# Performance work log

Hardware: AMD Instinct MI355X
Metric: run time of the kernel (lower is better)

The kernel has to match this reference:

```python
import jax, jax.numpy as jnp
import numpy as np

N, DN, DE, L, FE = 1024, 128, 128, 4, 5

def setup_inputs() -> dict:
    key = jax.random.key(0)
    ks = jax.random.split(key, 20)
    f = lambda k, shape, fan: jax.random.normal(k, shape, dtype=jnp.float32) / np.sqrt(fan)
    h = jax.random.normal(ks[0], (1, N, DN), dtype=jnp.float32)
    e = jax.random.normal(ks[1], (1, N, N, DE), dtype=jnp.float32)
    adj = (jax.random.uniform(ks[2], (1, N, N)) < 0.03).astype(jnp.float32)  # sparse-ish dense adjacency
    edge = jax.random.normal(ks[3], (FE,), dtype=jnp.float32)
    return {
        'h': h, 'e': e, 'adj': adj, 'edge': edge,
        # message linear over concat(h_j, e_ij), split into node/edge parts
        'w_msg_h': f(ks[4], (DN, DN), DN + DE),
        'w_msg_e': f(ks[5], (DN, DE), DN + DE),
        'b_msg':   jnp.zeros((DN,), jnp.float32),
        # GRUCell params (torch layout: gates r,z,n stacked)
        'w_ih': f(ks[6], (3 * DN, DN), DN),
        'w_hh': f(ks[7], (3 * DN, DN), DN),
        'b_ih': jnp.zeros((3 * DN,), jnp.float32),
        'b_hh': jnp.zeros((3 * DN,), jnp.float32),
        # gated-sum readout to graph vector of size DE
        'w_gate': f(ks[8], (DE, 2 * DN), 2 * DN),
        'b_gate': jnp.zeros((DE,), jnp.float32),
        'w_out':  f(ks[9], (DE, 2 * DN), 2 * DN),
        'b_out':  jnp.zeros((DE,), jnp.float32),
        # edge embedding (no bias) and final fc
        'w_embed': f(ks[10], (DE, FE), FE),
        'w_fc':    f(ks[11], (DE, 2 * DE), 2 * DE),
        'b_fc':    jnp.zeros((DE,), jnp.float32),
    }


def reference(h, e, adj, edge, w_msg_h, w_msg_e, b_msg, w_ih, w_hh, b_ih, b_hh,
              w_gate, b_gate, w_out, b_out, w_embed, w_fc, b_fc):
    h0 = h
    # edge part of the message is layer-independent: precompute once [1,N,N,DN]
    e_msg = jnp.einsum('bijf,df->bijd', e, w_msg_e)
    for _ in range(L):
        # m_i = sum_j adj_ij * (W_h h_j + W_e e_ij) + b
        m = (jnp.einsum('bij,bjd->bid', adj, h @ w_msg_h.T)
             + jnp.einsum('bij,bijd->bid', adj, e_msg) + b_msg)
        gi = m @ w_ih.T + b_ih
        gh = h @ w_hh.T + b_hh
        gir, giz, gin = jnp.split(gi, 3, axis=-1)
        ghr, ghz, ghn = jnp.split(gh, 3, axis=-1)
        r = jax.nn.sigmoid(gir + ghr)
        z = jax.nn.sigmoid(giz + ghz)
        n = jnp.tanh(gin + r * ghn)
        h = (1.0 - z) * n + z * h
    # gated-sum readout over nodes -> graph vector [1, DE]
    hc = jnp.concatenate([h, h0], axis=-1)
    gv = jnp.sum(jax.nn.sigmoid(hc @ w_gate.T + b_gate) * jnp.tanh(hc @ w_out.T + b_out), axis=1)
    gv = gv.squeeze(0)                      # [DE]
    ee = w_embed @ edge                     # [DE]
    init_edge = jnp.concatenate([gv, ee], axis=-1) @ w_fc.T + b_fc  # [DE]
    return init_edge
```

## Files before the change

### kernel.cpp

```cpp
#include <hip/hip_runtime.h>


__device__ __forceinline__ float sigm(float x){ return 1.f / (1.f + __expf(-x)); }

constexpr int N = 1024, D = 128, CAP = 192;

constexpr int OFF_WT_ME   = 0;
constexpr int OFF_WT_IH   = OFF_WT_ME   + 128*128;
constexpr int OFF_WT_HH   = OFF_WT_IH   + 128*384;
constexpr int OFF_WT_GATE = OFF_WT_HH   + 128*384;
constexpr int OFF_WT_OUT  = OFF_WT_GATE + 256*128;
constexpr int OFF_WT_FC   = OFF_WT_OUT  + 256*128;
constexpr int OFF_EE      = OFF_WT_FC   + 256*128;
constexpr int OFF_GV      = OFF_EE + 128;
constexpr int OFF_WCT     = OFF_GV + 128;
constexpr int OFF_C       = OFF_WCT + 128*384;
constexpr int OFF_EC      = OFF_C   + N*384;
constexpr int OFF_HA      = OFF_EC  + N*D;
constexpr int OFF_HB      = OFF_HA  + N*D;
constexpr int OFF_CNT     = OFF_HB  + N*D;
constexpr int OFF_NZI     = OFF_CNT + N;
constexpr int OFF_NZV     = OFF_NZI + N*CAP;

constexpr int PT0 = OFF_WT_IH, PT1 = OFF_WT_HH, PT2 = OFF_WT_GATE, PT3 = OFF_WT_OUT,
              PT4 = OFF_WT_FC, PT5 = OFF_EE, PT6 = OFF_GV, PT7 = OFF_WCT;

__global__ __launch_bounds__(256)
void k_prep(const float* w_me, const float* w_ih, const float* w_hh,
            const float* w_gate, const float* w_out, const float* w_fc,
            const float* w_embed, const float* edge, float* ws){
  int idx = blockIdx.x * 256 + threadIdx.x;
  if (idx < PT0)      { int k = idx;       int f = k >> 7, d = k & 127; ws[idx] = w_me[d*128 + f]; }
  else if (idx < PT1) { int k = idx - PT0; int f = k / 384, o = k % 384; ws[idx] = w_ih[o*128 + f]; }
  else if (idx < PT2) { int k = idx - PT1; int f = k / 384, o = k % 384; ws[idx] = w_hh[o*128 + f]; }
  else if (idx < PT3) { int k = idx - PT2; int f = k >> 7, c = k & 127; ws[idx] = w_gate[c*256 + f]; }
  else if (idx < PT4) { int k = idx - PT3; int f = k >> 7, c = k & 127; ws[idx] = w_out[c*256 + f]; }
  else if (idx < PT5) { int k = idx - PT4; int c = k >> 7, o = k & 127; ws[idx] = w_fc[o*256 + c]; }
  else if (idx < PT6) { int c = idx - PT5; float a = 0.f;
                        for (int q = 0; q < 5; ++q) a += w_embed[c*5 + q] * edge[q];
                        ws[idx] = a; }
  else if (idx < PT7) { ws[idx] = 0.f; }
}

__global__ __launch_bounds__(128)
void k_wc(const float* w_ih, const float* w_mh, float* ws){
  __shared__ float ih_sh[128];
  const int o = blockIdx.x, t = threadIdx.x;
  ih_sh[t] = w_ih[o*128 + t];
  __syncthreads();
  float acc = 0.f;
  for (int d = 0; d < 128; ++d) acc += ih_sh[d] * w_mh[d*128 + t];
  ws[OFF_WCT + t*384 + o] = acc;
}

__global__ __launch_bounds__(256)
void k_gather(const float* adj, const float* e, const float* h, const float* b_msg, float* ws){
  __shared__ int   cnt_sh;
  __shared__ int   idx_sh[CAP];
  __shared__ float val_sh[CAP];
  __shared__ float red_sh[512];
  __shared__ float ea_sh[128];
  const int i = blockIdx.x, t = threadIdx.x;
  if (t == 0) cnt_sh = 0;
  __syncthreads();
  const float* arow = adj + (size_t)i * N;
  #pragma unroll
  for (int q = 0; q < 4; ++q){
    int j = t + q*256;
    float v = arow[j];
    if (v != 0.f){
      int p = atomicAdd(&cnt_sh, 1);
      if (p < CAP){ idx_sh[p] = j; val_sh[p] = v; }
    }
  }
  __syncthreads();
  const int cnt = min(cnt_sh, CAP);
  int*   cntp = (int*)(ws + OFF_CNT);
  int*   nzi  = (int*)(ws + OFF_NZI);
  float* nzv  = ws + OFF_NZV;
  if (t == 0) cntp[i] = cnt;
  for (int k = t; k < cnt; k += 256){ nzi[(size_t)i*CAP + k] = idx_sh[k]; nzv[(size_t)i*CAP + k] = val_sh[k]; }

  const int lane = t & 63, wv = t >> 6;
  float ax = 0.f, ay = 0.f;
  const float* eb = e + ((size_t)i << 17);
  for (int k = wv; k < cnt; k += 4){
    int j = idx_sh[k]; float v = val_sh[k];
    float2 uu = *(const float2*)(eb + (size_t)j*128 + 2*lane);
    ax += v * uu.x;
    ay += v * uu.y;
  }
  red_sh[wv*128 + 2*lane]     = ax;
  red_sh[wv*128 + 2*lane + 1] = ay;
  __syncthreads();
  if (t < 128) ea_sh[t] = red_sh[t] + red_sh[128+t] + red_sh[256+t] + red_sh[384+t];
  __syncthreads();

  const float* wT = ws + OFF_WT_ME;
  const int d = t & 127, half = t >> 7;
  float acc = 0.f;
  for (int f = half*64; f < half*64 + 64; ++f) acc += ea_sh[f] * wT[f*128 + d];
  red_sh[half*128 + d] = acc;
  __syncthreads();
  if (t < 128){
    ws[OFF_EC + (size_t)i*128 + t] = red_sh[t] + red_sh[128 + t] + b_msg[t];
    ws[OFF_HA + (size_t)i*128 + t] = h[(size_t)i*128 + t];
  }
}

__global__ __launch_bounds__(384)
void k_cprep(const float* b_ih, float* ws){
  __shared__ float ec_sh[4][128];
  const int t = threadIdx.x, i0 = blockIdx.x * 4;
  const float* ec = ws + OFF_EC;
  for (int idx = t; idx < 512; idx += 384){
    int n = idx >> 7, c = idx & 127;
    ec_sh[n][c] = ec[(size_t)(i0+n)*128 + c];
  }
  __syncthreads();
  const float* wi_ = ws + OFF_WT_IH;
  float acc[4] = {};
  for (int f = 0; f < 128; ++f){
    float w = wi_[f*384 + t];
    #pragma unroll
    for (int n = 0; n < 4; ++n) acc[n] += w * ec_sh[n][f];
  }
  const float bi = b_ih[t];
  float* C = ws + OFF_C;
  #pragma unroll
  for (int n = 0; n < 4; ++n) C[(size_t)(i0+n)*384 + t] = acc[n] + bi;
}

__global__ __launch_bounds__(384)
void k_layer(const float* b_hh, const float* hA, float* hB, float* ws){
  __shared__ float hs_sh[4][128], h_sh[4][128];
  __shared__ float sr_sh[4][128], sz_sh[4][128], gn_sh[4][128], hn_sh[4][128];
  const int t = threadIdx.x, i0 = blockIdx.x * 4;
  const int*   cntp = (const int*)(ws + OFF_CNT);
  const int*   nzi  = (const int*)(ws + OFF_NZI);
  const float* nzv  = ws + OFF_NZV;
  for (int idx = t; idx < 512; idx += 384){
    int n = idx >> 7, c = idx & 127, i = i0 + n;
    h_sh[n][c] = hA[(size_t)i*128 + c];
    float a = 0.f;
    const int cn = cntp[i];
    const int*   ji = nzi + (size_t)i*CAP;
    const float* jv = nzv + (size_t)i*CAP;
    for (int k = 0; k < cn; ++k) a += jv[k] * hA[(size_t)ji[k]*128 + c];
    hs_sh[n][c] = a;
  }
  __syncthreads();
  const float* wc_ = ws + OFF_WCT;
  const float* wh_ = ws + OFF_WT_HH;
  float ag[4] = {}, ah[4] = {};
  for (int f = 0; f < 128; ++f){
    float wi = wc_[f*384 + t], wh = wh_[f*384 + t];
    #pragma unroll
    for (int n = 0; n < 4; ++n){ ag[n] += wi * hs_sh[n][f]; ah[n] += wh * h_sh[n][f]; }
  }
  const float* C = ws + OFF_C;
  float cv[4];
  #pragma unroll
  for (int n = 0; n < 4; ++n) cv[n] = C[(size_t)(i0+n)*384 + t];
  const float bh = b_hh[t];
  if (t < 128){
    #pragma unroll
    for (int n = 0; n < 4; ++n) sr_sh[n][t] = ag[n] + cv[n] + ah[n] + bh;
  } else if (t < 256){
    const int c = t - 128;
    #pragma unroll
    for (int n = 0; n < 4; ++n) sz_sh[n][c] = ag[n] + cv[n] + ah[n] + bh;
  } else {
    const int c = t - 256;
    #pragma unroll
    for (int n = 0; n < 4; ++n){ gn_sh[n][c] = ag[n] + cv[n]; hn_sh[n][c] = ah[n] + bh; }
  }
  __syncthreads();
  for (int idx = t; idx < 512; idx += 384){
    int n = idx >> 7, c = idx & 127;
    float r  = sigm(sr_sh[n][c]);
    float z  = sigm(sz_sh[n][c]);
    float nn = tanhf(gn_sh[n][c] + r * hn_sh[n][c]);
    hB[(size_t)(i0+n)*128 + c] = (1.f - z) * nn + z * h_sh[n][c];
  }
}

__global__ __launch_bounds__(128)
void k_readout(const float* h0, const float* b_gate, const float* b_out, float* ws){
  __shared__ float hc_sh[8][256];
  const int t = threadIdx.x, i0 = blockIdx.x * 8;
  const float* hcur = ws + OFF_HA;
  #pragma unroll
  for (int n = 0; n < 8; ++n){
    hc_sh[n][t]       = hcur[(size_t)(i0+n)*128 + t];
    hc_sh[n][128 + t] = h0[(size_t)(i0+n)*128 + t];
  }
  __syncthreads();
  const float* wg_ = ws + OFF_WT_GATE;
  const float* wo_ = ws + OFF_WT_OUT;
  float ag[8] = {}, ao[8] = {};
  for (int f = 0; f < 256; ++f){
    float wg = wg_[f*128 + t], wo = wo_[f*128 + t];
    #pragma unroll
    for (int n = 0; n < 8; ++n){ ag[n] += wg * hc_sh[n][f]; ao[n] += wo * hc_sh[n][f]; }
  }
  const float bg = b_gate[t], bo = b_out[t];
  float s = 0.f;
  #pragma unroll
  for (int n = 0; n < 8; ++n) s += sigm(ag[n] + bg) * tanhf(ao[n] + bo);
  atomicAdd(ws + OFF_GV + t, s);
}

__global__ __launch_bounds__(128)
void k_fc(const float* b_fc, float* out, const float* ws){
  const int o = threadIdx.x;
  const float* wT = ws + OFF_WT_FC;
  const float* gv = ws + OFF_GV;
  const float* ee = ws + OFF_EE;
  float acc = b_fc[o];
  for (int c = 0; c < 128; ++c) acc += gv[c] * wT[c*128 + o];
  for (int c = 0; c < 128; ++c) acc += ee[c] * wT[(128 + c)*128 + o];
  out[o] = acc;
}

extern "C" void kernel_launch(void* const* d_in, const int* in_sizes, int n_in,
                              void* d_out, int out_size, void* d_ws, size_t ws_size,
                              hipStream_t stream){
  const float* h      = (const float*)d_in[0];
  const float* e      = (const float*)d_in[1];
  const float* adj    = (const float*)d_in[2];
  const float* edge   = (const float*)d_in[3];
  const float* w_mh   = (const float*)d_in[4];
  const float* w_me   = (const float*)d_in[5];
  const float* b_msg  = (const float*)d_in[6];
  const float* w_ih   = (const float*)d_in[7];
  const float* w_hh   = (const float*)d_in[8];
  const float* b_ih   = (const float*)d_in[9];
  const float* b_hh   = (const float*)d_in[10];
  const float* w_gate = (const float*)d_in[11];
  const float* b_gate = (const float*)d_in[12];
  const float* w_out  = (const float*)d_in[13];
  const float* b_out  = (const float*)d_in[14];
  const float* w_emb  = (const float*)d_in[15];
  const float* w_fc   = (const float*)d_in[16];
  const float* b_fc   = (const float*)d_in[17];
  float* ws = (float*)d_ws;

  k_prep<<<(PT7 + 255) / 256, 256, 0, stream>>>(w_me, w_ih, w_hh, w_gate, w_out,
                                                w_fc, w_emb, edge, ws);
  k_wc<<<384, 128, 0, stream>>>(w_ih, w_mh, ws);
  k_gather<<<N, 256, 0, stream>>>(adj, e, h, b_msg, ws);
  k_cprep<<<N/4, 384, 0, stream>>>(b_ih, ws);
  float* hA = ws + OFF_HA;
  float* hB = ws + OFF_HB;
  for (int l = 0; l < 4; ++l){
    const float* src = (l & 1) ? hB : hA;
    float*       dst = (l & 1) ? hA : hB;
    k_layer<<<N/4, 384, 0, stream>>>(b_hh, src, dst, ws);
  }
  k_readout<<<N/8, 128, 0, stream>>>(h, b_gate, b_out, ws);
  k_fc<<<1, 128, 0, stream>>>(b_fc, (float*)d_out, ws);
}
```

Measured before the change: 789.0 us.

## Fuse all stages into one cooperative persistent kernel with grid syncs

Replaces the chain of separate launches (prep, weight combine, gather, C precompute, four GRU layers, readout, fc) with a single cooperative kernel of 256 blocks that keeps the adjacency nonzero lists, edge aggregates and input-gate precompute in shared memory and uses grid.sync between layers. It removes launch overhead and global round-trips for intermediates such as C, EC and the nonzero index lists. In exchange, the edge gather that dominates runtime now runs on only 256 blocks of 384 threads instead of 1024 blocks, which reduces parallelism for the memory-bound e-tensor reads. It also relies on every block being co-resident for the grid barriers.

```diff
diff --git a/kernel.cpp b/kernel.cpp
--- a/kernel.cpp
+++ b/kernel.cpp
@@ -1,9 +1,13 @@
 #include <hip/hip_runtime.h>
-
+#include <hip/hip_cooperative_groups.h>
+
+
+namespace cg = cooperative_groups;
 
 __device__ __forceinline__ float sigm(float x){ return 1.f / (1.f + __expf(-x)); }
 
-constexpr int N = 1024, D = 128, CAP = 192;
+constexpr int N = 1024, CAP = 192;
+constexpr int NB = 256, NT = 384;
 
 constexpr int OFF_WT_ME   = 0;
 constexpr int OFF_WT_IH   = OFF_WT_ME   + 128*128;
@@ -14,213 +18,214 @@
 constexpr int OFF_EE      = OFF_WT_FC   + 256*128;
 constexpr int OFF_GV      = OFF_EE + 128;
 constexpr int OFF_WCT     = OFF_GV + 128;
-constexpr int OFF_C       = OFF_WCT + 128*384;
-constexpr int OFF_EC      = OFF_C   + N*384;
-constexpr int OFF_HA      = OFF_EC  + N*D;
-constexpr int OFF_HB      = OFF_HA  + N*D;
-constexpr int OFF_CNT     = OFF_HB  + N*D;
-constexpr int OFF_NZI     = OFF_CNT + N;
-constexpr int OFF_NZV     = OFF_NZI + N*CAP;
+constexpr int OFF_HA      = OFF_WCT + 128*384;
+constexpr int OFF_HB      = OFF_HA  + N*128;
 
 constexpr int PT0 = OFF_WT_IH, PT1 = OFF_WT_HH, PT2 = OFF_WT_GATE, PT3 = OFF_WT_OUT,
               PT4 = OFF_WT_FC, PT5 = OFF_EE, PT6 = OFF_GV, PT7 = OFF_WCT;
 
-__global__ __launch_bounds__(256)
-void k_prep(const float* w_me, const float* w_ih, const float* w_hh,
-            const float* w_gate, const float* w_out, const float* w_fc,
-            const float* w_embed, const float* edge, float* ws){
-  int idx = blockIdx.x * 256 + threadIdx.x;
-  if (idx < PT0)      { int k = idx;       int f = k >> 7, d = k & 127; ws[idx] = w_me[d*128 + f]; }
-  else if (idx < PT1) { int k = idx - PT0; int f = k / 384, o = k % 384; ws[idx] = w_ih[o*128 + f]; }
-  else if (idx < PT2) { int k = idx - PT1; int f = k / 384, o = k % 384; ws[idx] = w_hh[o*128 + f]; }
-  else if (idx < PT3) { int k = idx - PT2; int f = k >> 7, c = k & 127; ws[idx] = w_gate[c*256 + f]; }
-  else if (idx < PT4) { int k = idx - PT3; int f = k >> 7, c = k & 127; ws[idx] = w_out[c*256 + f]; }
-  else if (idx < PT5) { int k = idx - PT4; int c = k >> 7, o = k & 127; ws[idx] = w_fc[o*256 + c]; }
-  else if (idx < PT6) { int c = idx - PT5; float a = 0.f;
-                        for (int q = 0; q < 5; ++q) a += w_embed[c*5 + q] * edge[q];
-                        ws[idx] = a; }
-  else if (idx < PT7) { ws[idx] = 0.f; }
-}
-
-__global__ __launch_bounds__(128)
-void k_wc(const float* w_ih, const float* w_mh, float* ws){
-  __shared__ float ih_sh[128];
-  const int o = blockIdx.x, t = threadIdx.x;
-  ih_sh[t] = w_ih[o*128 + t];
+__global__ __launch_bounds__(NT, 1)
+void k_mega(const float* __restrict__ h,    const float* __restrict__ e,
+            const float* __restrict__ adj,
+            const float* __restrict__ w_mh, const float* __restrict__ w_me,
+            const float* __restrict__ b_msg,
+            const float* __restrict__ w_ih, const float* __restrict__ w_hh,
+            const float* __restrict__ b_ih, const float* __restrict__ b_hh,
+            const float* __restrict__ w_gate, const float* __restrict__ b_gate,
+            const float* __restrict__ w_out,  const float* __restrict__ b_out,
+            const float* __restrict__ w_emb,  const float* __restrict__ edge,
+            const float* __restrict__ w_fc,   const float* __restrict__ b_fc,
+            float* __restrict__ out, float* ws){
+  cg::grid_group grid = cg::this_grid();
+  const int t = threadIdx.x, b = blockIdx.x, i0 = b * 4;
+
+  __shared__ int   idxs[4][CAP];
+  __shared__ float vals[4][CAP];
+  __shared__ int   cnta[4];
+  __shared__ int   cnt_cur;
+  __shared__ float ea_sh[4][128];
+  __shared__ float red_sh[6*128];
+  __shared__ float ih_sh[3][128];
+  __shared__ float ec_sh[4][128];
+  __shared__ float hs_sh[4][128], h_sh[4][128];
+  __shared__ float sr_sh[4][128], sz_sh[4][128], gn_sh[4][128], hn_sh[4][128];
+
+  for (int idx = b*NT + t; idx < PT7; idx += NB*NT){
+    if (idx < PT0)      { int k = idx;       int f = k >> 7, d = k & 127; ws[idx] = w_me[d*128 + f]; }
+    else if (idx < PT1) { int k = idx - PT0; int f = k / 384, o = k % 384; ws[idx] = w_ih[o*128 + f]; }
+    else if (idx < PT2) { int k = idx - PT1; int f = k / 384, o = k % 384; ws[idx] = w_hh[o*128 + f]; }
+    else if (idx < PT3) { int k = idx - PT2; int f = k >> 7, c = k & 127; ws[idx] = w_gate[c*256 + f]; }
+    else if (idx < PT4) { int k = idx - PT3; int f = k >> 7, c = k & 127; ws[idx] = w_out[c*256 + f]; }
+    else if (idx < PT5) { int k = idx - PT4; int c = k >> 7, o = k & 127; ws[idx] = w_fc[o*256 + c]; }
+    else if (idx < PT6) { int c = idx - PT5; float a = 0.f;
+                          for (int q = 0; q < 5; ++q) a += w_emb[c*5 + q] * edge[q];
+                          ws[idx] = a; }
+    else                { ws[idx] = 0.f; }
+  }
+
+  if (b < 128){
+    const int g = t >> 7, f = t & 127, o = b*3 + g;
+    ih_sh[g][f] = w_ih[o*128 + f];
+    __syncthreads();
+    float acc = 0.f;
+    for (int d = 0; d < 128; ++d) acc += ih_sh[g][d] * w_mh[d*128 + f];
+    ws[OFF_WCT + f*384 + o] = acc;
+  }
+
+  const int lane = t & 63, wv = t >> 6;
+  for (int n = 0; n < 4; ++n){
+    const int i = i0 + n;
+    if (t == 0) cnt_cur = 0;
+    __syncthreads();
+    const float* arow = adj + (size_t)i * N;
+    for (int j = t; j < N; j += NT){
+      float v = arow[j];
+      if (v != 0.f){
+        int p = atomicAdd(&cnt_cur, 1);
+        if (p < CAP){ idxs[n][p] = j; vals[n][p] = v; }
+      }
+    }
+    __syncthreads();
+    const int cnt = min(cnt_cur, CAP);
+    if (t == 0) cnta[n] = cnt;
+    float ax = 0.f, ay = 0.f;
+    const float* eb = e + ((size_t)i << 17);
+    for (int k = wv; k < cnt; k += 6){
+      int j = idxs[n][k]; float v = vals[n][k];
+      float2 uu = *(const float2*)(eb + (size_t)j*128 + 2*lane);
+      ax += v * uu.x;
+      ay += v * uu.y;
+    }
+    red_sh[wv*128 + 2*lane]     = ax;
+    red_sh[wv*128 + 2*lane + 1] = ay;
+    __syncthreads();
+    if (t < 128){
+      float s = red_sh[t];
+      #pragma unroll
+      for (int w = 1; w < 6; ++w) s += red_sh[w*128 + t];
+      ea_sh[n][t] = s;
+    }
+    __syncthreads();
+  }
+  grid.sync();
+
+  {
+    const float* wT = ws + OFF_WT_ME;
+    for (int idx = t; idx < 512; idx += NT){
+      const int n = idx >> 7, d = idx & 127;
+      float acc = 0.f;
+      for (int f = 0; f < 128; ++f) acc += ea_sh[n][f] * wT[f*128 + d];
+      ec_sh[n][d] = acc + b_msg[d];
+    }
+  }
   __syncthreads();
-  float acc = 0.f;
-  for (int d = 0; d < 128; ++d) acc += ih_sh[d] * w_mh[d*128 + t];
-  ws[OFF_WCT + t*384 + o] = acc;
-}
-
-__global__ __launch_bounds__(256)
-void k_gather(const float* adj, const float* e, const float* h, const float* b_msg, float* ws){
-  __shared__ int   cnt_sh;
-  __shared__ int   idx_sh[CAP];
-  __shared__ float val_sh[CAP];
-  __shared__ float red_sh[512];
-  __shared__ float ea_sh[128];
-  const int i = blockIdx.x, t = threadIdx.x;
-  if (t == 0) cnt_sh = 0;
+  float cv[4];
+  {
+    const float* wi_ = ws + OFF_WT_IH;
+    float a0=0.f, a1=0.f, a2=0.f, a3=0.f;
+    for (int f = 0; f < 128; ++f){
+      const float w = wi_[f*384 + t];
+      a0 += w*ec_sh[0][f]; a1 += w*ec_sh[1][f]; a2 += w*ec_sh[2][f]; a3 += w*ec_sh[3][f];
+    }
+    const float bi = b_ih[t];
+    cv[0]=a0+bi; cv[1]=a1+bi; cv[2]=a2+bi; cv[3]=a3+bi;
+  }
+  const float bh = b_hh[t];
+
+  float* hA = ws + OFF_HA;
+  float* hB = ws + OFF_HB;
+  const float* wc_ = ws + OFF_WCT;
+  const float* wh_ = ws + OFF_WT_HH;
+
+  for (int l = 0; l < 4; ++l){
+    const float* src = (l == 0) ? h : ((l & 1) ? hA : hB);
+    float* dst = (l & 1) ? hB : hA;
+    for (int idx = t; idx < 512; idx += NT){
+      const int n = idx >> 7, c = idx & 127;
+      h_sh[n][c] = src[(size_t)(i0+n)*128 + c];
+      float a = 0.f;
+      const int cn = cnta[n];
+      for (int k = 0; k < cn; ++k) a += vals[n][k] * src[(size_t)idxs[n][k]*128 + c];
+      hs_sh[n][c] = a;
+    }
+    __syncthreads();
+    float ag[4] = {}, ah[4] = {};
+    for (int f = 0; f < 128; ++f){
+      const float wi = wc_[f*384 + t], wh = wh_[f*384 + t];
+      #pragma unroll
+      for (int n = 0; n < 4; ++n){ ag[n] += wi*hs_sh[n][f]; ah[n] += wh*h_sh[n][f]; }
+    }
+    if (t < 128){
+      #pragma unroll
+      for (int n = 0; n < 4; ++n) sr_sh[n][t] = ag[n] + cv[n] + ah[n] + bh;
+    } else if (t < 256){
+      const int c = t - 128;
+      #pragma unroll
+      for (int n = 0; n < 4; ++n) sz_sh[n][c] = ag[n] + cv[n] + ah[n] + bh;
+    } else {
+      const int c = t - 256;
+      #pragma unroll
+      for (int n = 0; n < 4; ++n){ gn_sh[n][c] = ag[n] + cv[n]; hn_sh[n][c] = ah[n] + bh; }
+    }
+    __syncthreads();
+    for (int idx = t; idx < 512; idx += NT){
+      const int n = idx >> 7, c = idx & 127;
+      float r  = sigm(sr_sh[n][c]);
+      float z  = sigm(sz_sh[n][c]);
+      float nn = tanhf(gn_sh[n][c] + r * hn_sh[n][c]);
+      float hv = (1.f - z) * nn + z * h_sh[n][c];
+      if (l < 3) dst[(size_t)(i0+n)*128 + c] = hv;
+      else       hs_sh[n][c] = hv;
+    }
+    if (l < 3) grid.sync();
+    else       __syncthreads();
+  }
+
+  for (int idx = t; idx < 512; idx += NT){
+    const int n = idx >> 7, c = idx & 127;
+    h_sh[n][c] = h[(size_t)(i0+n)*128 + c];
+  }
   __syncthreads();
-  const float* arow = adj + (size_t)i * N;
-  #pragma unroll
-  for (int q = 0; q < 4; ++q){
-    int j = t + q*256;
-    float v = arow[j];
-    if (v != 0.f){
-      int p = atomicAdd(&cnt_sh, 1);
-      if (p < CAP){ idx_sh[p] = j; val_sh[p] = v; }
-    }
-  }
-  __syncthreads();
-  const int cnt = min(cnt_sh, CAP);
-  int*   cntp = (int*)(ws + OFF_CNT);
-  int*   nzi  = (int*)(ws + OFF_NZI);
-  float* nzv  = ws + OFF_NZV;
-  if (t == 0) cntp[i] = cnt;
-  for (int k = t; k < cnt; k += 256){ nzi[(size_t)i*CAP + k] = idx_sh[k]; nzv[(size_t)i*CAP + k] = val_sh[k]; }
-
-  const int lane = t & 63, wv = t >> 6;
-  float ax = 0.f, ay = 0.f;
-  const float* eb = e + ((size_t)i << 17);
-  for (int k = wv; k < cnt; k += 4){
-    int j = idx_sh[k]; float v = val_sh[k];
-    float2 uu = *(const float2*)(eb + (size_t)j*128 + 2*lane);
-    ax += v * uu.x;
-    ay += v * uu.y;
-  }
-  red_sh[wv*128 + 2*lane]     = ax;
-  red_sh[wv*128 + 2*lane + 1] = ay;
-  __syncthreads();
-  if (t < 128) ea_sh[t] = red_sh[t] + red_sh[128+t] + red_sh[256+t] + red_sh[384+t];
-  __syncthreads();
-
-  const float* wT = ws + OFF_WT_ME;
-  const int d = t & 127, half = t >> 7;
-  float acc = 0.f;
-  for (int f = half*64; f < half*64 + 64; ++f) acc += ea_sh[f] * wT[f*128 + d];
-  red_sh[half*128 + d] = acc;
+  {
+    const float* wg_ = ws + OFF_WT_GATE;
+    const float* wo_ = ws + OFF_WT_OUT;
+    if (t < 256){
+      const int c = t & 127;
+      const float* wm = (t < 128) ? wg_ : wo_;
+      float a[4] = {};
+      for (int f = 0; f < 128; ++f){
+        const float w0 = wm[f*128 + c], w1 = wm[(128+f)*128 + c];
+        #pragma unroll
+        for (int n = 0; n < 4; ++n) a[n] += hs_sh[n][f]*w0 + h_sh[n][f]*w1;
+      }
+      if (t < 128){
+        #pragma unroll
+        for (int n = 0; n < 4; ++n) sz_sh[n][c] = a[n];
+      } else {
+        #pragma unroll
+        for (int n = 0; n < 4; ++n) gn_sh[n][c] = a[n];
+      }
+    }
+  }
   __syncthreads();
   if (t < 128){
-    ws[OFF_EC + (size_t)i*128 + t] = red_sh[t] + red_sh[128 + t] + b_msg[t];
-    ws[OFF_HA + (size_t)i*128 + t] = h[(size_t)i*128 + t];
-  }
-}
-
-__global__ __launch_bounds__(384)
-void k_cprep(const float* b_ih, float* ws){
-  __shared__ float ec_sh[4][128];
-  const int t = threadIdx.x, i0 = blockIdx.x * 4;
-  const float* ec = ws + OFF_EC;
-  for (int idx = t; idx < 512; idx += 384){
-    int n = idx >> 7, c = idx & 127;
-    ec_sh[n][c] = ec[(size_t)(i0+n)*128 + c];
-  }
-  __syncthreads();
-  const float* wi_ = ws + OFF_WT_IH;
-  float acc[4] = {};
-  for (int f = 0; f < 128; ++f){
-    float w = wi_[f*384 + t];
+    const float bg = b_gate[t], bo = b_out[t];
+    float s = 0.f;
     #pragma unroll
-    for (int n = 0; n < 4; ++n) acc[n] += w * ec_sh[n][f];
-  }
-  const float bi = b_ih[t];
-  float* C = ws + OFF_C;
-  #pragma unroll
-  for (int n = 0; n < 4; ++n) C[(size_t)(i0+n)*384 + t] = acc[n] + bi;
-}
-
-__global__ __launch_bounds__(384)
-void k_layer(const float* b_hh, const float* hA, float* hB, float* ws){
-  __shared__ float hs_sh[4][128], h_sh[4][128];
-  __shared__ float sr_sh[4][128], sz_sh[4][128], gn_sh[4][128], hn_sh[4][128];
-  const int t = threadIdx.x, i0 = blockIdx.x * 4;
-  const int*   cntp = (const int*)(ws + OFF_CNT);
-  const int*   nzi  = (const int*)(ws + OFF_NZI);
-  const float* nzv  = ws + OFF_NZV;
-  for (int idx = t; idx < 512; idx += 384){
-    int n = idx >> 7, c = idx & 127, i = i0 + n;
-    h_sh[n][c] = hA[(size_t)i*128 + c];
-    float a = 0.f;
-    const int cn = cntp[i];
-    const int*   ji = nzi + (size_t)i*CAP;
-    const float* jv = nzv + (size_t)i*CAP;
-    for (int k = 0; k < cn; ++k) a += jv[k] * hA[(size_t)ji[k]*128 + c];
-    hs_sh[n][c] = a;
-  }
-  __syncthreads();
-  const float* wc_ = ws + OFF_WCT;
-  const float* wh_ = ws + OFF_WT_HH;
-  float ag[4] = {}, ah[4] = {};
-  for (int f = 0; f < 128; ++f){
-    float wi = wc_[f*384 + t], wh = wh_[f*384 + t];
-    #pragma unroll
-    for (int n = 0; n < 4; ++n){ ag[n] += wi * hs_sh[n][f]; ah[n] += wh * h_sh[n][f]; }
-  }
-  const float* C = ws + OFF_C;
-  float cv[4];
-  #pragma unroll
-  for (int n = 0; n < 4; ++n) cv[n] = C[(size_t)(i0+n)*384 + t];
-  const float bh = b_hh[t];
-  if (t < 128){
-    #pragma unroll
-    for (int n = 0; n < 4; ++n) sr_sh[n][t] = ag[n] + cv[n] + ah[n] + bh;
-  } else if (t < 256){
-    const int c = t - 128;
-    #pragma unroll
-    for (int n = 0; n < 4; ++n) sz_sh[n][c] = ag[n] + cv[n] + ah[n] + bh;
-  } else {
-    const int c = t - 256;
-    #pragma unroll
-    for (int n = 0; n < 4; ++n){ gn_sh[n][c] = ag[n] + cv[n]; hn_sh[n][c] = ah[n] + bh; }
-  }
-  __syncthreads();
-  for (int idx = t; idx < 512; idx += 384){
-    int n = idx >> 7, c = idx & 127;
-    float r  = sigm(sr_sh[n][c]);
-    float z  = sigm(sz_sh[n][c]);
-    float nn = tanhf(gn_sh[n][c] + r * hn_sh[n][c]);
-    hB[(size_t)(i0+n)*128 + c] = (1.f - z) * nn + z * h_sh[n][c];
-  }
-}
-
-__global__ __launch_bounds__(128)
-void k_readout(const float* h0, const float* b_gate, const float* b_out, float* ws){
-  __shared__ float hc_sh[8][256];
-  const int t = threadIdx.x, i0 = blockIdx.x * 8;
-  const float* hcur = ws + OFF_HA;
-  #pragma unroll
-  for (int n = 0; n < 8; ++n){
-    hc_sh[n][t]       = hcur[(size_t)(i0+n)*128 + t];
-    hc_sh[n][128 + t] = h0[(size_t)(i0+n)*128 + t];
-  }
-  __syncthreads();
-  const float* wg_ = ws + OFF_WT_GATE;
-  const float* wo_ = ws + OFF_WT_OUT;
-  float ag[8] = {}, ao[8] = {};
-  for (int f = 0; f < 256; ++f){
-    float wg = wg_[f*128 + t], wo = wo_[f*128 + t];
-    #pragma unroll
-    for (int n = 0; n < 8; ++n){ ag[n] += wg * hc_sh[n][f]; ao[n] += wo * hc_sh[n][f]; }
-  }
-  const float bg = b_gate[t], bo = b_out[t];
-  float s = 0.f;
-  #pragma unroll
-  for (int n = 0; n < 8; ++n) s += sigm(ag[n] + bg) * tanhf(ao[n] + bo);
-  atomicAdd(ws + OFF_GV + t, s);
-}
-
-__global__ __launch_bounds__(128)
-void k_fc(const float* b_fc, float* out, const float* ws){
-  const int o = threadIdx.x;
-  const float* wT = ws + OFF_WT_FC;
-  const float* gv = ws + OFF_GV;
-  const float* ee = ws + OFF_EE;
-  float acc = b_fc[o];
-  for (int c = 0; c < 128; ++c) acc += gv[c] * wT[c*128 + o];
-  for (int c = 0; c < 128; ++c) acc += ee[c] * wT[(128 + c)*128 + o];
-  out[o] = acc;
+    for (int n = 0; n < 4; ++n) s += sigm(sz_sh[n][t] + bg) * tanhf(gn_sh[n][t] + bo);
+    atomicAdd(ws + OFF_GV + t, s);
+  }
+  grid.sync();
+
+  if (b == 0 && t < 128){
+    const float* wT = ws + OFF_WT_FC;
+    const float* gv = ws + OFF_GV;
+    const float* ee = ws + OFF_EE;
+    float acc = b_fc[t];
+    for (int c = 0; c < 128; ++c) acc += gv[c] * wT[c*128 + t];
+    for (int c = 0; c < 128; ++c) acc += ee[c] * wT[(128 + c)*128 + t];
+    out[t] = acc;
+  }
 }
 
 extern "C" void kernel_launch(void* const* d_in, const int* in_sizes, int n_in,
@@ -244,20 +249,14 @@
   const float* w_emb  = (const float*)d_in[15];
   const float* w_fc   = (const float*)d_in[16];
   const float* b_fc   = (const float*)d_in[17];
-  float* ws = (float*)d_ws;
-
-  k_prep<<<(PT7 + 255) / 256, 256, 0, stream>>>(w_me, w_ih, w_hh, w_gate, w_out,
-                                                w_fc, w_emb, edge, ws);
-  k_wc<<<384, 128, 0, stream>>>(w_ih, w_mh, ws);
-  k_gather<<<N, 256, 0, stream>>>(adj, e, h, b_msg, ws);
-  k_cprep<<<N/4, 384, 0, stream>>>(b_ih, ws);
-  float* hA = ws + OFF_HA;
-  float* hB = ws + OFF_HB;
-  for (int l = 0; l < 4; ++l){
-    const float* src = (l & 1) ? hB : hA;
-    float*       dst = (l & 1) ? hA : hB;
-    k_layer<<<N/4, 384, 0, stream>>>(b_hh, src, dst, ws);
-  }
-  k_readout<<<N/8, 128, 0, stream>>>(h, b_gate, b_out, ws);
-  k_fc<<<1, 128, 0, stream>>>(b_fc, (float*)d_out, ws);
+  float* outp = (float*)d_out;
+  float* ws   = (float*)d_ws;
+
+  void* args[] = { (void*)&h, (void*)&e, (void*)&adj,
+                   (void*)&w_mh, (void*)&w_me, (void*)&b_msg,
+                   (void*)&w_ih, (void*)&w_hh, (void*)&b_ih, (void*)&b_hh,
+                   (void*)&w_gate, (void*)&b_gate, (void*)&w_out, (void*)&b_out,
+                   (void*)&w_emb, (void*)&edge, (void*)&w_fc, (void*)&b_fc,
+                   (void*)&outp, (void*)&ws };
+  hipLaunchCooperativeKernel((void*)k_mega, dim3(NB), dim3(NT), args, 0, stream);
 }
```

Measured after the change: 915.2 us. 16.0% more time.
